# Kernel optimization log

Hardware: AMD Instinct MI355X
Metric: run time of the kernel (lower is better)

Reference implementation:

```python
import jax, jax.numpy as jnp
import numpy as np

B, V, L, H, E, META = 2048, 4096, 10, 512, 256, 15
TAU = 1.2
SOS = 0
EOS = 0


def setup_inputs() -> dict:
    key = jax.random.key(0)
    ks = jax.random.split(key, 8)
    hidden_state = jax.random.normal(ks[0], (B, META), jnp.float32)
    W_in = jax.random.normal(ks[1], (META, H), jnp.float32) * 0.1
    b_in = jnp.zeros((H,), jnp.float32)
    embedding = jax.random.normal(ks[2], (V, E), jnp.float32) * 0.1
    W_ih = jax.random.normal(ks[3], (4 * H, E), jnp.float32) * (1.0 / np.sqrt(E))
    W_hh = jax.random.normal(ks[4], (4 * H, H), jnp.float32) * (1.0 / np.sqrt(H))
    b_ih = jnp.zeros((4 * H,), jnp.float32)
    # forget-gate bias initialized to 1 (reset_parameters)
    b_hh = jnp.zeros((4 * H,), jnp.float32).at[H:2 * H].set(1.0)
    W_out = jax.random.normal(ks[5], (H, V), jnp.float32) * 0.02
    b_out = jnp.zeros((V,), jnp.float32)
    u = jax.random.uniform(ks[6], (L, B, V), jnp.float32, 1e-8, 1.0 - 1e-8)
    gumbel = -jnp.log(-jnp.log(u))
    return {"hidden_state": hidden_state, "W_in": W_in, "b_in": b_in,
            "embedding": embedding, "W_ih": W_ih, "W_hh": W_hh,
            "b_ih": b_ih, "b_hh": b_hh, "W_out": W_out, "b_out": b_out,
            "gumbel": gumbel}


def reference(hidden_state, W_in, b_in, embedding, W_ih, W_hh, b_ih, b_hh,
              W_out, b_out, gumbel):
    initial_length = L + 1
    h0 = hidden_state @ W_in + b_in              # [B,H] input_module (meta)
    c0 = jnp.zeros_like(h0)
    tok0 = jnp.zeros((B, V), jnp.float32).at[:, SOS].set(1.0)  # one-hot sos
    sl0 = jnp.full((B,), initial_length, jnp.int32)

    def step(carry, xs):
        h, c, tok, sl = carry
        i, g = xs
        emb = tok @ embedding                                  # [B,E]
        gates = emb @ W_ih.T + b_ih + h @ W_hh.T + b_hh        # [B,4H]
        ig, fg, gg, og = jnp.split(gates, 4, axis=1)
        c = jax.nn.sigmoid(fg) * c + jax.nn.sigmoid(ig) * jnp.tanh(gg)
        h = jax.nn.sigmoid(og) * jnp.tanh(c)
        logits = h @ W_out + b_out                             # [B,V]
        logp = jax.nn.log_softmax(logits, axis=1)
        p = jnp.exp(logp)
        ent = -jnp.sum(p * logp, axis=1)                       # Categorical entropy
        # gumbel_softmax(p, tau, hard=True): softmax((log p + g)/tau), straight-through
        y = jax.nn.softmax((logp + g) / TAU, axis=1)
        hard = jax.nn.one_hot(jnp.argmax(y, axis=1), V, dtype=y.dtype)
        tok_new = jax.lax.stop_gradient(hard - y) + y
        mask = (hard[:, EOS] == 1.0) & (sl == initial_length)
        sl = jnp.where(mask, i + 2, sl)  # seq_pos = i+1, set to seq_pos+1
        return (h, c, tok_new, sl), (tok_new, emb, ent)

    (_, _, _, seq_lengths), (toks, embeds, ents) = jax.lax.scan(
        step, (h0, c0, tok0, sl0), (jnp.arange(L, dtype=jnp.int32), gumbel))
    output = jnp.concatenate([tok0[:, None, :], jnp.transpose(toks, (1, 0, 2))], axis=1)  # [B,L+1,V]
    embeds_out = jnp.transpose(embeds, (1, 0, 2))              # [B,L,E]
    entropy = jnp.mean(jnp.sum(ents, axis=0)) / L
    sentence_probability = jnp.zeros((B, V), jnp.float32)      # only filled in eval mode
    return output, seq_lengths, entropy, embeds_out, sentence_probability
```

## Files before the change

kernel.cpp:

```cpp
#include <hip/hip_runtime.h>
#include <hip/hip_bf16.h>
#include <math.h>

typedef unsigned short u16;
typedef __attribute__((ext_vector_type(8))) short bf16x8;
typedef __attribute__((ext_vector_type(4))) float f32x4;

#define B_    2048
#define V_    4096
#define L_    10
#define H_    512
#define E_    256
#define META_ 15
#define H4_   2048
#define W6_   (H4_ + V_)
#define EOS_  0
#define INIT_LEN_ (L_ + 1)

constexpr size_t OUT_SL  = (size_t)B_ * (L_ + 1) * V_;
constexpr size_t OUT_ENT = OUT_SL + B_;
constexpr size_t OUT_EMB = OUT_ENT + 1;
constexpr size_t OUT_SP  = OUT_EMB + (size_t)B_ * L_ * E_;

constexpr size_t WS_E2G     = 0;
constexpr size_t WS_LOGITS  = WS_E2G    + (size_t)V_ * H4_;
constexpr size_t WS_G       = WS_LOGITS + (size_t)B_ * V_;
constexpr size_t WS_C       = WS_G      + (size_t)B_ * H4_;
constexpr size_t WS_F32_END = WS_C      + (size_t)B_ * H_;
constexpr size_t U_W6_HI    = 0;
constexpr size_t U_W6_LO    = U_W6_HI + (size_t)W6_ * H_;
constexpr size_t U_HHI      = U_W6_LO + (size_t)W6_ * H_;
constexpr size_t U_HLO      = U_HHI   + (size_t)B_ * H_;
constexpr size_t U_END      = U_HLO   + (size_t)B_ * H_;

__device__ __forceinline__ u16 f2bf(float f) {
    union { __hip_bfloat16 b; u16 u; } cv; cv.b = __float2bfloat16(f); return cv.u;
}
__device__ __forceinline__ float bf2f(u16 u) {
    union { u16 u; __hip_bfloat16 b; } cv; cv.u = u; return __bfloat162float(cv.b);
}

__device__ __forceinline__ void gld16(const u16* g, void* l) {
    __builtin_amdgcn_global_load_lds(
        (const __attribute__((address_space(1))) unsigned int*)g,
        (__attribute__((address_space(3))) unsigned int*)l, 16, 0, 0);
}

template <int EPI>
__global__ __launch_bounds__(256)
void gemm3(const u16* __restrict__ Ah, const u16* __restrict__ Al,
           const u16* __restrict__ Bh, const u16* __restrict__ Bl,
           float* __restrict__ C0, float* __restrict__ C1, int K,
           const float* __restrict__ bias0, const float* __restrict__ bias1,
           int xoff)
{
    __shared__ u16 As[2][128][32];
    __shared__ u16 Bs[2][128][32];
    const int tid  = threadIdx.x;
    const int lane = tid & 63;
    const int wave = tid >> 6;
    const int wm = wave >> 1, wn = wave & 1;

    const int nwg  = gridDim.x * gridDim.y;
    const int bid  = blockIdx.y * gridDim.x + blockIdx.x;
    const int w    = (bid & 7) * (nwg >> 3) + (bid >> 3);
    const int colb = w / gridDim.y + xoff;
    const int rowb = w % gridDim.y;
    const int col0 = colb * 128;
    const int row0 = rowb * 128;

    const int srow = tid >> 2;
    const int scol = (tid & 3) * 8;
    const size_t aoff = (size_t)(row0 + srow) * K + scol;
    const size_t boff = (size_t)(col0 + srow) * K + scol;
    const size_t skip = (size_t)64 * K;

    u16* lA0 = &As[0][0][0];
    u16* lA1 = &As[1][0][0];
    u16* lB0 = &Bs[0][0][0];
    u16* lB1 = &Bs[1][0][0];
    const int d0 = tid * 8;
    const int d1 = d0 + 2048;

    f32x4 acc[4][4] = {};
    const int fr = lane & 15;
    const int kq = lane >> 4;

    for (int k0 = 0; k0 < K; k0 += 32) {
        __syncthreads();
        gld16(Ah + aoff + k0,        lA0 + d0);
        gld16(Ah + aoff + k0 + skip, lA0 + d1);
        gld16(Al + aoff + k0,        lA1 + d0);
        gld16(Al + aoff + k0 + skip, lA1 + d1);
        gld16(Bh + boff + k0,        lB0 + d0);
        gld16(Bh + boff + k0 + skip, lB0 + d1);
        gld16(Bl + boff + k0,        lB1 + d0);
        gld16(Bl + boff + k0 + skip, lB1 + d1);
        __syncthreads();

        bf16x8 ah[4], al[4], bh[4], bl[4];
#pragma unroll
        for (int i = 0; i < 4; ++i) {
            ah[i] = *(const bf16x8*)&As[0][wm * 64 + i * 16 + fr][kq * 8];
            al[i] = *(const bf16x8*)&As[1][wm * 64 + i * 16 + fr][kq * 8];
            bh[i] = *(const bf16x8*)&Bs[0][wn * 64 + i * 16 + fr][kq * 8];
            bl[i] = *(const bf16x8*)&Bs[1][wn * 64 + i * 16 + fr][kq * 8];
        }
#pragma unroll
        for (int mi = 0; mi < 4; ++mi)
#pragma unroll
            for (int ni = 0; ni < 4; ++ni) {
                acc[mi][ni] = __builtin_amdgcn_mfma_f32_16x16x32_bf16(ah[mi], bh[ni], acc[mi][ni], 0, 0, 0);
                acc[mi][ni] = __builtin_amdgcn_mfma_f32_16x16x32_bf16(ah[mi], bl[ni], acc[mi][ni], 0, 0, 0);
                acc[mi][ni] = __builtin_amdgcn_mfma_f32_16x16x32_bf16(al[mi], bh[ni], acc[mi][ni], 0, 0, 0);
            }
    }

    const int cc0 = col0 + wn * 64 + fr;
    float* Cbase;
    int ldc, ccol;
    bool addBias;
    if (EPI == 0) {
        Cbase = C0; ldc = H4_; ccol = cc0; addBias = true;
    } else {
        const bool isG = (col0 < H4_);
        Cbase = isG ? C0 : C1;
        ldc   = isG ? H4_ : V_;
        ccol  = isG ? cc0 : cc0 - H4_;
        addBias = !isG;
    }
#pragma unroll
    for (int mi = 0; mi < 4; ++mi) {
#pragma unroll
        for (int r = 0; r < 4; ++r) {
            const int grow = row0 + wm * 64 + mi * 16 + kq * 4 + r;
            float* cp = Cbase + (size_t)grow * ldc + ccol;
#pragma unroll
            for (int ni = 0; ni < 4; ++ni) {
                float v = acc[mi][ni][r];
                if (EPI == 0) v += bias0[ccol + ni * 16] + bias1[ccol + ni * 16];
                if (EPI == 1 && addBias) v += bias0[ccol + ni * 16];
                cp[ni * 16] = v;
            }
        }
    }
}

__global__ __launch_bounds__(256)
void split_wout(const float* __restrict__ W_out, u16* __restrict__ hiT,
                u16* __restrict__ loT)
{
    __shared__ float t[32][33];
    const int v0 = blockIdx.x * 32, k0 = blockIdx.y * 32;
    const int x = threadIdx.x & 31, y = threadIdx.x >> 5;
    for (int yy = y; yy < 32; yy += 8)
        t[yy][x] = W_out[(size_t)(k0 + yy) * V_ + v0 + x];
    __syncthreads();
    for (int yy = y; yy < 32; yy += 8) {
        const float v = t[x][yy];
        const u16 h = f2bf(v);
        hiT[(size_t)(v0 + yy) * H_ + k0 + x] = h;
        loT[(size_t)(v0 + yy) * H_ + k0 + x] = f2bf(v - bf2f(h));
    }
}

__global__ __launch_bounds__(256)
void split_mat(const float* __restrict__ X, u16* __restrict__ hi,
               u16* __restrict__ lo)
{
    const int i = blockIdx.x * 256 + threadIdx.x;
    float4 v = ((const float4*)X)[i];
    const u16 h0 = f2bf(v.x), h1 = f2bf(v.y), h2 = f2bf(v.z), h3 = f2bf(v.w);
    ((ushort4*)hi)[i] = make_ushort4(h0, h1, h2, h3);
    ((ushort4*)lo)[i] = make_ushort4(f2bf(v.x - bf2f(h0)), f2bf(v.y - bf2f(h1)),
                                     f2bf(v.z - bf2f(h2)), f2bf(v.w - bf2f(h3)));
}

__global__ __launch_bounds__(256)
void h0_kernel(const float* __restrict__ hs, const float* __restrict__ W_in,
               const float* __restrict__ b_in, u16* __restrict__ h_hi,
               u16* __restrict__ h_lo, float* __restrict__ c)
{
    const int idx = blockIdx.x * 256 + threadIdx.x;
    const int b = idx >> 9, j = idx & 511;
    float acc = b_in[j];
#pragma unroll
    for (int e = 0; e < META_; ++e)
        acc = fmaf(hs[b * META_ + e], W_in[e * H_ + j], acc);
    const u16 hh = f2bf(acc);
    h_hi[idx] = hh;
    h_lo[idx] = f2bf(acc - bf2f(hh));
    c[idx] = 0.f;
}

__global__ __launch_bounds__(256)
void init_outputs(float* __restrict__ out, int* __restrict__ tok,
                  int* __restrict__ sl, float* __restrict__ ents)
{
    const int tid = blockIdx.x * 256 + threadIdx.x;
    {
        const int b = tid >> 10;
        const int q = tid & 1023;
        float4 z = make_float4(0.f, 0.f, 0.f, 0.f);
        if (q == 0) z.x = 1.0f;
        ((float4*)out)[(size_t)b * ((L_ + 1) * V_ / 4) + q] = z;
    }
    for (size_t t = tid; t < (size_t)B_ * V_; t += (size_t)gridDim.x * 256)
        out[OUT_SP + t] = 0.f;
    if (tid < B_) { tok[tid] = 0; sl[tid] = INIT_LEN_; ents[tid] = 0.f; }
}

__global__ __launch_bounds__(256)
void lstm_cell(const float* __restrict__ G, const float* __restrict__ e2g,
               u16* __restrict__ h_hi, u16* __restrict__ h_lo,
               float* __restrict__ c, const float* __restrict__ embedding,
               const int* __restrict__ tok, float* __restrict__ out, int step)
{
    const int idx = blockIdx.x * 256 + threadIdx.x;
    const int b = idx >> 9, j = idx & 511;
    const size_t g0 = (size_t)b * H4_;
    const size_t e0 = (size_t)tok[b] * H4_;
    const float ig = G[g0 + j]          + e2g[e0 + j];
    const float fg = G[g0 + H_ + j]     + e2g[e0 + H_ + j];
    const float gg = G[g0 + 2 * H_ + j] + e2g[e0 + 2 * H_ + j];
    const float og = G[g0 + 3 * H_ + j] + e2g[e0 + 3 * H_ + j];
    const float si = 1.f / (1.f + expf(-ig));
    const float sf = 1.f / (1.f + expf(-fg));
    const float so = 1.f / (1.f + expf(-og));
    const float cn = sf * c[idx] + si * tanhf(gg);
    c[idx] = cn;
    const float hv = so * tanhf(cn);
    const u16 hh = f2bf(hv);
    h_hi[idx] = hh;
    h_lo[idx] = f2bf(hv - bf2f(hh));
    if (j < E_)
        out[OUT_EMB + ((size_t)b * L_ + step) * E_ + j] =
            embedding[(size_t)tok[b] * E_ + j];
}

__global__ __launch_bounds__(256)
void softmax_step(const float* __restrict__ logits, const float* __restrict__ gumbel,
                  float* __restrict__ out, int* __restrict__ tok,
                  int* __restrict__ sl, float* __restrict__ ents, int step)
{
    const int b   = blockIdx.x;
    const int tid = threadIdx.x;
    const float* lrow = logits + (size_t)b * V_;
    const float* grow = gumbel + ((size_t)step * B_ + b) * V_;
    __shared__ float lsm[V_];
    __shared__ float red_m[4], red_bv[4], red_s[4], red_t[4];
    __shared__ int   red_bi[4];
    __shared__ float s_M;
    __shared__ int   s_bi;

    float m = -3.4e38f, bv = -3.4e38f;
    int bi = 0x7fffffff;
    for (int q = tid; q < V_ / 4; q += 256) {
        float4 l4 = ((const float4*)lrow)[q];
        float4 g4 = ((const float4*)grow)[q];
        ((float4*)lsm)[q] = l4;
        m = fmaxf(m, fmaxf(fmaxf(l4.x, l4.y), fmaxf(l4.z, l4.w)));
        float p; const int i4 = q * 4;
        p = l4.x + g4.x; if (p > bv) { bv = p; bi = i4; }
        p = l4.y + g4.y; if (p > bv) { bv = p; bi = i4 + 1; }
        p = l4.z + g4.z; if (p > bv) { bv = p; bi = i4 + 2; }
        p = l4.w + g4.w; if (p > bv) { bv = p; bi = i4 + 3; }
    }
#pragma unroll
    for (int off = 32; off > 0; off >>= 1) {
        m = fmaxf(m, __shfl_down(m, off));
        float obv = __shfl_down(bv, off);
        int   obi = __shfl_down(bi, off);
        if (obv > bv || (obv == bv && obi < bi)) { bv = obv; bi = obi; }
    }
    const int wave = tid >> 6, lane = tid & 63;
    if (lane == 0) { red_m[wave] = m; red_bv[wave] = bv; red_bi[wave] = bi; }
    __syncthreads();
    if (tid == 0) {
        m = red_m[0]; bv = red_bv[0]; bi = red_bi[0];
        for (int w = 1; w < 4; ++w) {
            m = fmaxf(m, red_m[w]);
            if (red_bv[w] > bv || (red_bv[w] == bv && red_bi[w] < bi)) {
                bv = red_bv[w]; bi = red_bi[w];
            }
        }
        s_M = m; s_bi = bi;
    }
    __syncthreads();
    const float M = s_M;
    const int amax = s_bi;

    float s = 0.f, t = 0.f;
    for (int q = tid; q < V_; q += 256) {
        const float l = lsm[q];
        const float e = __expf(l - M);
        s += e; t += e * l;
    }
#pragma unroll
    for (int off = 32; off > 0; off >>= 1) {
        s += __shfl_down(s, off);
        t += __shfl_down(t, off);
    }
    if (lane == 0) { red_s[wave] = s; red_t[wave] = t; }

    float* orow = out + ((size_t)b * (L_ + 1) + step + 1) * V_;
    const float4 z4 = make_float4(0.f, 0.f, 0.f, 0.f);
    for (int q = tid; q < V_ / 4; q += 256) ((float4*)orow)[q] = z4;
    __syncthreads();
    if (tid == 0) {
        const float ss = red_s[0] + red_s[1] + red_s[2] + red_s[3];
        const float tt = red_t[0] + red_t[1] + red_t[2] + red_t[3];
        const float ent = (M + logf(ss)) - tt / ss;
        ents[b] += ent;
        orow[amax] = 1.0f;
        tok[b] = amax;
        if (amax == EOS_ && sl[b] == INIT_LEN_) sl[b] = step + 2;
    }
}

__global__ __launch_bounds__(256)
void finalize(const int* __restrict__ sl, const float* __restrict__ ents,
              float* __restrict__ out)
{
    const int tid = threadIdx.x;
    float s = 0.f;
    for (int b = tid; b < B_; b += 256) {
        s += ents[b];
        out[OUT_SL + b] = (float)sl[b];
    }
    __shared__ float red[4];
#pragma unroll
    for (int off = 32; off > 0; off >>= 1) s += __shfl_down(s, off);
    if ((tid & 63) == 0) red[tid >> 6] = s;
    __syncthreads();
    if (tid == 0)
        out[OUT_ENT] = (red[0] + red[1] + red[2] + red[3]) / (float)B_ / (float)L_;
}

extern "C" void kernel_launch(void* const* d_in, const int* in_sizes, int n_in,
                              void* d_out, int out_size, void* d_ws, size_t ws_size,
                              hipStream_t stream)
{
    const float* hidden    = (const float*)d_in[0];
    const float* W_in      = (const float*)d_in[1];
    const float* b_in      = (const float*)d_in[2];
    const float* embedding = (const float*)d_in[3];
    const float* W_ih      = (const float*)d_in[4];
    const float* W_hh      = (const float*)d_in[5];
    const float* b_ih      = (const float*)d_in[6];
    const float* b_hh      = (const float*)d_in[7];
    const float* W_out     = (const float*)d_in[8];
    const float* b_out     = (const float*)d_in[9];
    const float* gumbel    = (const float*)d_in[10];
    float* out = (float*)d_out;

    float* ws    = (float*)d_ws;
    float* E2G   = ws + WS_E2G;
    float* logit = ws + WS_LOGITS;
    float* G     = ws + WS_G;
    float* c     = ws + WS_C;
    u16*   wsu   = (u16*)(ws + WS_F32_END);
    u16* w6_hi   = wsu + U_W6_HI;
    u16* w6_lo   = wsu + U_W6_LO;
    u16* h_hi    = wsu + U_HHI;
    u16* h_lo    = wsu + U_HLO;
    int* tok     = (int*)(wsu + U_END);
    int* sl      = tok + B_;
    float* ents  = (float*)(sl + B_);
    u16* emb_hi  = (u16*)logit;
    u16* emb_lo  = emb_hi + (size_t)V_ * E_;
    u16* wih_hi  = emb_lo + (size_t)V_ * E_;
    u16* wih_lo  = wih_hi + (size_t)H4_ * E_;

    split_mat<<<(H4_ * H_ / 4) / 256, 256, 0, stream>>>(W_hh, w6_hi, w6_lo);
    split_wout<<<dim3(V_ / 32, H_ / 32), 256, 0, stream>>>(
        W_out, w6_hi + (size_t)H4_ * H_, w6_lo + (size_t)H4_ * H_);
    split_mat<<<(V_ * E_ / 4) / 256, 256, 0, stream>>>(embedding, emb_hi, emb_lo);
    split_mat<<<(H4_ * E_ / 4) / 256, 256, 0, stream>>>(W_ih, wih_hi, wih_lo);
    h0_kernel<<<(B_ * H_) / 256, 256, 0, stream>>>(hidden, W_in, b_in, h_hi, h_lo, c);
    init_outputs<<<(B_ * V_ / 4) / 256, 256, 0, stream>>>(out, tok, sl, ents);
    gemm3<0><<<dim3(H4_ / 128, V_ / 128), 256, 0, stream>>>(
        emb_hi, emb_lo, wih_hi, wih_lo, E2G, nullptr, E_, b_ih, b_hh, 0);
    gemm3<1><<<dim3(H4_ / 128, B_ / 128), 256, 0, stream>>>(
        h_hi, h_lo, w6_hi, w6_lo, G, logit, H_, b_out, nullptr, 0);

    for (int i = 0; i < L_; ++i) {
        lstm_cell<<<(B_ * H_) / 256, 256, 0, stream>>>(G, E2G, h_hi, h_lo, c,
                                                       embedding, tok, out, i);
        if (i < L_ - 1) {
            gemm3<1><<<dim3(W6_ / 128, B_ / 128), 256, 0, stream>>>(
                h_hi, h_lo, w6_hi, w6_lo, G, logit, H_, b_out, nullptr, 0);
        } else {
            gemm3<1><<<dim3(V_ / 128, B_ / 128), 256, 0, stream>>>(
                h_hi, h_lo, w6_hi, w6_lo, G, logit, H_, b_out, nullptr, H4_ / 128);
        }
        softmax_step<<<B_, 256, 0, stream>>>(logit, gumbel, out, tok, sl, ents, i);
    }
    finalize<<<1, 256, 0, stream>>>(sl, ents, out);
}
```

Measured before the change: 865.1 us.

## Replace split-bf16 GEMM with 256x256-tile kernel over concatenated hi/lo K dimension

```diff
diff --git a/kernel.cpp b/kernel.cpp
--- a/kernel.cpp
+++ b/kernel.cpp
@@ -13,7 +13,8 @@
 #define E_    256
 #define META_ 15
 #define H4_   2048
-#define W6_   (H4_ + V_)
+#define KT_   1536
+#define NT_   48
 #define EOS_  0
 #define INIT_LEN_ (L_ + 1)
 
@@ -27,11 +28,9 @@
 constexpr size_t WS_G       = WS_LOGITS + (size_t)B_ * V_;
 constexpr size_t WS_C       = WS_G      + (size_t)B_ * H4_;
 constexpr size_t WS_F32_END = WS_C      + (size_t)B_ * H_;
-constexpr size_t U_W6_HI    = 0;
-constexpr size_t U_W6_LO    = U_W6_HI + (size_t)W6_ * H_;
-constexpr size_t U_HHI      = U_W6_LO + (size_t)W6_ * H_;
-constexpr size_t U_HLO      = U_HHI   + (size_t)B_ * H_;
-constexpr size_t U_END      = U_HLO   + (size_t)B_ * H_;
+constexpr size_t U_B6       = 0;
+constexpr size_t U_HP       = U_B6 + (size_t)6144 * KT_;
+constexpr size_t U_END      = U_HP + (size_t)B_ * KT_;
 
 __device__ __forceinline__ u16 f2bf(float f) {
     union { __hip_bfloat16 b; u16 u; } cv; cv.b = __float2bfloat16(f); return cv.u;
@@ -39,11 +38,164 @@
 __device__ __forceinline__ float bf2f(u16 u) {
     union { u16 u; __hip_bfloat16 b; } cv; cv.u = u; return __bfloat162float(cv.b);
 }
-
 __device__ __forceinline__ void gld16(const u16* g, void* l) {
     __builtin_amdgcn_global_load_lds(
         (const __attribute__((address_space(1))) unsigned int*)g,
         (__attribute__((address_space(3))) unsigned int*)l, 16, 0, 0);
+}
+
+__device__ __forceinline__ size_t b6_addr(int col, int k) {
+    const int p = col >> 8, row = col & 255, kt = k >> 5, s = (k >> 3) & 3, e = k & 7;
+    return (size_t)(p * NT_ + kt) * 8192 + s * 2048 + row * 8 + e;
+}
+
+__global__ __launch_bounds__(512, 1)
+void gemm8(const u16* __restrict__ Ag, const u16* __restrict__ B6,
+           float* __restrict__ G, float* __restrict__ LOG,
+           const float* __restrict__ bias, int xoff)
+{
+    __shared__ u16 As[2][8192];
+    __shared__ u16 Bs[2][8192];
+    const int tid  = threadIdx.x;
+    const int lane = tid & 63;
+    const int wave = tid >> 6;
+    const int wr = wave >> 2, wc = wave & 3;
+    const int fr = lane & 15, kq = lane >> 4;
+
+    const int nwg = gridDim.x * gridDim.y;
+    const int bid = blockIdx.y * gridDim.x + blockIdx.x;
+    const int w   = (bid & 7) * (nwg >> 3) + (bid >> 3);
+    const int colb = (w >> 3) + xoff;
+    const int row0 = (w & 7) * 256;
+    const int col0 = colb * 256;
+
+    const u16* Asrc = Ag + (size_t)(row0 + (tid & 255)) * KT_ + (tid >> 8) * 8;
+    const u16* Bsrc = B6 + (size_t)colb * (NT_ * 8192) + tid * 8;
+    const int dst0 = tid * 8;
+
+    const int abase = kq * 2048 + (wr * 128 + fr) * 8;
+    const int bbase = kq * 2048 + (wc * 64 + fr) * 8;
+
+    f32x4 acc[8][4] = {};
+    bf16x8 aF[8], bF[4], aN[8], bN[4];
+
+#define STAGE(buf, kt) do {                                    \
+    gld16(Asrc + (kt) * 32,        &As[buf][dst0]);            \
+    gld16(Asrc + (kt) * 32 + 16,   &As[buf][dst0 + 4096]);     \
+    gld16(Bsrc + (kt) * 8192,        &Bs[buf][dst0]);          \
+    gld16(Bsrc + (kt) * 8192 + 4096, &Bs[buf][dst0 + 4096]);   \
+  } while (0)
+
+    STAGE(0, 0);
+    STAGE(1, 1);
+    asm volatile("s_waitcnt vmcnt(4)\ns_barrier" ::: "memory");
+    {
+        const u16* ap = &As[0][abase];
+        const u16* bp = &Bs[0][bbase];
+#pragma unroll
+        for (int m = 0; m < 8; ++m) aF[m] = *(const bf16x8*)(ap + m * 128);
+#pragma unroll
+        for (int n = 0; n < 4; ++n) bF[n] = *(const bf16x8*)(bp + n * 128);
+    }
+
+#define BODY(T, AF, BF, AN, BN) do {                                          \
+    const int cur = (T) & 1;                                                  \
+    __builtin_amdgcn_s_setprio(1);                                            \
+    _Pragma("unroll")                                                         \
+    for (int m = 0; m < 8; ++m) {                                             \
+      acc[m][0] = __builtin_amdgcn_mfma_f32_16x16x32_bf16(AF[m], BF[0], acc[m][0], 0, 0, 0); \
+      acc[m][1] = __builtin_amdgcn_mfma_f32_16x16x32_bf16(AF[m], BF[1], acc[m][1], 0, 0, 0); \
+    }                                                                         \
+    __builtin_amdgcn_s_setprio(0);                                            \
+    asm volatile("s_waitcnt lgkmcnt(0)\ns_barrier" ::: "memory");             \
+    { int t2 = (T) + 2; if (t2 >= NT_) t2 = (T);                              \
+      STAGE(cur, t2); }                                                       \
+    __builtin_amdgcn_s_setprio(1);                                            \
+    _Pragma("unroll")                                                         \
+    for (int m = 0; m < 8; ++m)                                               \
+      acc[m][2] = __builtin_amdgcn_mfma_f32_16x16x32_bf16(AF[m], BF[2], acc[m][2], 0, 0, 0); \
+    __builtin_amdgcn_s_setprio(0);                                            \
+    asm volatile("s_waitcnt vmcnt(4)\ns_barrier" ::: "memory");               \
+    { const u16* ap = &As[cur ^ 1][abase];                                    \
+      const u16* bp = &Bs[cur ^ 1][bbase];                                    \
+      _Pragma("unroll")                                                       \
+      for (int m = 0; m < 8; ++m) AN[m] = *(const bf16x8*)(ap + m * 128);     \
+      _Pragma("unroll")                                                       \
+      for (int n = 0; n < 4; ++n) BN[n] = *(const bf16x8*)(bp + n * 128); }   \
+    __builtin_amdgcn_s_setprio(1);                                            \
+    _Pragma("unroll")                                                         \
+    for (int m = 0; m < 8; ++m)                                               \
+      acc[m][3] = __builtin_amdgcn_mfma_f32_16x16x32_bf16(AF[m], BF[3], acc[m][3], 0, 0, 0); \
+    __builtin_amdgcn_s_setprio(0);                                            \
+  } while (0)
+
+    for (int t = 0; t < NT_; t += 2) {
+        BODY(t,     aF, bF, aN, bN);
+        BODY(t + 1, aN, bN, aF, bF);
+    }
+#undef BODY
+#undef STAGE
+
+    const bool isG = (col0 < H4_);
+    float* Cb   = isG ? G : LOG;
+    const int ldc  = isG ? H4_ : V_;
+    const int cadj = isG ? 0 : H4_;
+    const int cbase = col0 - cadj + wc * 64 + fr;
+#pragma unroll
+    for (int m = 0; m < 8; ++m) {
+#pragma unroll
+        for (int r = 0; r < 4; ++r) {
+            const int grow = row0 + wr * 128 + m * 16 + kq * 4 + r;
+            float* cp = Cb + (size_t)grow * ldc + cbase;
+#pragma unroll
+            for (int n = 0; n < 4; ++n) {
+                float v = acc[m][n][r];
+                if (!isG) v += bias[cbase + n * 16];
+                cp[n * 16] = v;
+            }
+        }
+    }
+}
+
+__global__ __launch_bounds__(256)
+void repack_whh(const float* __restrict__ W_hh, u16* __restrict__ B6)
+{
+    const int c0 = blockIdx.x * 32, k0 = blockIdx.y * 64;
+    const int cc = threadIdx.x & 31, kg = threadIdx.x >> 5;
+    const int col = c0 + cc;
+#pragma unroll
+    for (int e = 0; e < 8; ++e) {
+        const int kp = k0 + kg * 8 + e;
+        const float v = W_hh[(size_t)col * H_ + kp];
+        const u16 h = f2bf(v);
+        const u16 l = f2bf(v - bf2f(h));
+        B6[b6_addr(col, kp)]          = h;
+        B6[b6_addr(col, 512 + kp)]    = h;
+        B6[b6_addr(col, 1024 + kp)]   = l;
+    }
+}
+
+__global__ __launch_bounds__(256)
+void repack_wout(const float* __restrict__ W_out, u16* __restrict__ B6)
+{
+    __shared__ float t[64][33];
+    const int c0 = blockIdx.x * 32, k0 = blockIdx.y * 64;
+    const int x = threadIdx.x & 31, y = threadIdx.x >> 5;
+    for (int yy = y; yy < 64; yy += 8)
+        t[yy][x] = W_out[(size_t)(k0 + yy) * V_ + c0 + x];
+    __syncthreads();
+    const int cc = threadIdx.x & 31, kg = threadIdx.x >> 5;
+    const int col = 2048 + c0 + cc;
+#pragma unroll
+    for (int e = 0; e < 8; ++e) {
+        const int kp = k0 + kg * 8 + e;
+        const float v = t[kp - k0][cc];
+        const u16 h = f2bf(v);
+        const u16 l = f2bf(v - bf2f(h));
+        B6[b6_addr(col, kp)]        = h;
+        B6[b6_addr(col, 512 + kp)]  = h;
+        B6[b6_addr(col, 1024 + kp)] = l;
+    }
 }
 
 template <int EPI>
@@ -60,7 +212,6 @@
     const int lane = tid & 63;
     const int wave = tid >> 6;
     const int wm = wave >> 1, wn = wave & 1;
-
     const int nwg  = gridDim.x * gridDim.y;
     const int bid  = blockIdx.y * gridDim.x + blockIdx.x;
     const int w    = (bid & 7) * (nwg >> 3) + (bid >> 3);
@@ -117,50 +268,16 @@
     }
 
     const int cc0 = col0 + wn * 64 + fr;
-    float* Cbase;
-    int ldc, ccol;
-    bool addBias;
-    if (EPI == 0) {
-        Cbase = C0; ldc = H4_; ccol = cc0; addBias = true;
-    } else {
-        const bool isG = (col0 < H4_);
-        Cbase = isG ? C0 : C1;
-        ldc   = isG ? H4_ : V_;
-        ccol  = isG ? cc0 : cc0 - H4_;
-        addBias = !isG;
-    }
 #pragma unroll
     for (int mi = 0; mi < 4; ++mi) {
 #pragma unroll
         for (int r = 0; r < 4; ++r) {
             const int grow = row0 + wm * 64 + mi * 16 + kq * 4 + r;
-            float* cp = Cbase + (size_t)grow * ldc + ccol;
-#pragma unroll
-            for (int ni = 0; ni < 4; ++ni) {
-                float v = acc[mi][ni][r];
-                if (EPI == 0) v += bias0[ccol + ni * 16] + bias1[ccol + ni * 16];
-                if (EPI == 1 && addBias) v += bias0[ccol + ni * 16];
-                cp[ni * 16] = v;
-            }
+            float* cp = C0 + (size_t)grow * H4_ + cc0;
+#pragma unroll
+            for (int ni = 0; ni < 4; ++ni)
+                cp[ni * 16] = acc[mi][ni][r] + bias0[cc0 + ni * 16] + bias1[cc0 + ni * 16];
         }
-    }
-}
-
-__global__ __launch_bounds__(256)
-void split_wout(const float* __restrict__ W_out, u16* __restrict__ hiT,
-                u16* __restrict__ loT)
-{
-    __shared__ float t[32][33];
-    const int v0 = blockIdx.x * 32, k0 = blockIdx.y * 32;
-    const int x = threadIdx.x & 31, y = threadIdx.x >> 5;
-    for (int yy = y; yy < 32; yy += 8)
-        t[yy][x] = W_out[(size_t)(k0 + yy) * V_ + v0 + x];
-    __syncthreads();
-    for (int yy = y; yy < 32; yy += 8) {
-        const float v = t[x][yy];
-        const u16 h = f2bf(v);
-        hiT[(size_t)(v0 + yy) * H_ + k0 + x] = h;
-        loT[(size_t)(v0 + yy) * H_ + k0 + x] = f2bf(v - bf2f(h));
     }
 }
 
@@ -178,8 +295,8 @@
 
 __global__ __launch_bounds__(256)
 void h0_kernel(const float* __restrict__ hs, const float* __restrict__ W_in,
-               const float* __restrict__ b_in, u16* __restrict__ h_hi,
-               u16* __restrict__ h_lo, float* __restrict__ c)
+               const float* __restrict__ b_in, u16* __restrict__ hp,
+               float* __restrict__ c)
 {
     const int idx = blockIdx.x * 256 + threadIdx.x;
     const int b = idx >> 9, j = idx & 511;
@@ -188,8 +305,9 @@
     for (int e = 0; e < META_; ++e)
         acc = fmaf(hs[b * META_ + e], W_in[e * H_ + j], acc);
     const u16 hh = f2bf(acc);
-    h_hi[idx] = hh;
-    h_lo[idx] = f2bf(acc - bf2f(hh));
+    const u16 hl = f2bf(acc - bf2f(hh));
+    u16* row = hp + (size_t)b * KT_;
+    row[j] = hh; row[512 + j] = hl; row[1024 + j] = hh;
     c[idx] = 0.f;
 }
 
@@ -212,9 +330,9 @@
 
 __global__ __launch_bounds__(256)
 void lstm_cell(const float* __restrict__ G, const float* __restrict__ e2g,
-               u16* __restrict__ h_hi, u16* __restrict__ h_lo,
-               float* __restrict__ c, const float* __restrict__ embedding,
-               const int* __restrict__ tok, float* __restrict__ out, int step)
+               u16* __restrict__ hp, float* __restrict__ c,
+               const float* __restrict__ embedding, const int* __restrict__ tok,
+               float* __restrict__ out, int step)
 {
     const int idx = blockIdx.x * 256 + threadIdx.x;
     const int b = idx >> 9, j = idx & 511;
@@ -231,8 +349,9 @@
     c[idx] = cn;
     const float hv = so * tanhf(cn);
     const u16 hh = f2bf(hv);
-    h_hi[idx] = hh;
-    h_lo[idx] = f2bf(hv - bf2f(hh));
+    const u16 hl = f2bf(hv - bf2f(hh));
+    u16* row = hp + (size_t)b * KT_;
+    row[j] = hh; row[512 + j] = hl; row[1024 + j] = hh;
     if (j < E_)
         out[OUT_EMB + ((size_t)b * L_ + step) * E_ + j] =
             embedding[(size_t)tok[b] * E_ + j];
@@ -360,10 +479,8 @@
     float* G     = ws + WS_G;
     float* c     = ws + WS_C;
     u16*   wsu   = (u16*)(ws + WS_F32_END);
-    u16* w6_hi   = wsu + U_W6_HI;
-    u16* w6_lo   = wsu + U_W6_LO;
-    u16* h_hi    = wsu + U_HHI;
-    u16* h_lo    = wsu + U_HLO;
+    u16* B6      = wsu + U_B6;
+    u16* hp      = wsu + U_HP;
     int* tok     = (int*)(wsu + U_END);
     int* sl      = tok + B_;
     float* ents  = (float*)(sl + B_);
@@ -372,27 +489,23 @@
     u16* wih_hi  = emb_lo + (size_t)V_ * E_;
     u16* wih_lo  = wih_hi + (size_t)H4_ * E_;
 
-    split_mat<<<(H4_ * H_ / 4) / 256, 256, 0, stream>>>(W_hh, w6_hi, w6_lo);
-    split_wout<<<dim3(V_ / 32, H_ / 32), 256, 0, stream>>>(
-        W_out, w6_hi + (size_t)H4_ * H_, w6_lo + (size_t)H4_ * H_);
+    repack_whh<<<dim3(H4_ / 32, H_ / 64), 256, 0, stream>>>(W_hh, B6);
+    repack_wout<<<dim3(V_ / 32, H_ / 64), 256, 0, stream>>>(W_out, B6);
     split_mat<<<(V_ * E_ / 4) / 256, 256, 0, stream>>>(embedding, emb_hi, emb_lo);
     split_mat<<<(H4_ * E_ / 4) / 256, 256, 0, stream>>>(W_ih, wih_hi, wih_lo);
-    h0_kernel<<<(B_ * H_) / 256, 256, 0, stream>>>(hidden, W_in, b_in, h_hi, h_lo, c);
+    h0_kernel<<<(B_ * H_) / 256, 256, 0, stream>>>(hidden, W_in, b_in, hp, c);
     init_outputs<<<(B_ * V_ / 4) / 256, 256, 0, stream>>>(out, tok, sl, ents);
     gemm3<0><<<dim3(H4_ / 128, V_ / 128), 256, 0, stream>>>(
         emb_hi, emb_lo, wih_hi, wih_lo, E2G, nullptr, E_, b_ih, b_hh, 0);
-    gemm3<1><<<dim3(H4_ / 128, B_ / 128), 256, 0, stream>>>(
-        h_hi, h_lo, w6_hi, w6_lo, G, logit, H_, b_out, nullptr, 0);
+    gemm8<<<dim3(8, 8), 512, 0, stream>>>(hp, B6, G, logit, b_out, 0);
 
     for (int i = 0; i < L_; ++i) {
-        lstm_cell<<<(B_ * H_) / 256, 256, 0, stream>>>(G, E2G, h_hi, h_lo, c,
+        lstm_cell<<<(B_ * H_) / 256, 256, 0, stream>>>(G, E2G, hp, c,
                                                        embedding, tok, out, i);
         if (i < L_ - 1) {
-            gemm3<1><<<dim3(W6_ / 128, B_ / 128), 256, 0, stream>>>(
-                h_hi, h_lo, w6_hi, w6_lo, G, logit, H_, b_out, nullptr, 0);
+            gemm8<<<dim3(24, 8), 512, 0, stream>>>(hp, B6, G, logit, b_out, 0);
         } else {
-            gemm3<1><<<dim3(V_ / 128, B_ / 128), 256, 0, stream>>>(
-                h_hi, h_lo, w6_hi, w6_lo, G, logit, H_, b_out, nullptr, H4_ / 128);
+            gemm8<<<dim3(16, 8), 512, 0, stream>>>(hp, B6, G, logit, b_out, 8);
         }
         softmax_step<<<B_, 256, 0, stream>>>(logit, gumbel, out, tok, sl, ents, i);
     }
```

New measurement: 1.222 ms. 1.41x slower.

## Fuse softmax partial reductions into GEMM epilogue and merge with LSTM cell

Applied to the files above, without the earlier changes.

```diff
diff --git a/kernel.cpp b/kernel.cpp
--- a/kernel.cpp
+++ b/kernel.cpp
@@ -23,10 +23,10 @@
 constexpr size_t OUT_SP  = OUT_EMB + (size_t)B_ * L_ * E_;
 
 constexpr size_t WS_E2G     = 0;
-constexpr size_t WS_LOGITS  = WS_E2G    + (size_t)V_ * H4_;
-constexpr size_t WS_G       = WS_LOGITS + (size_t)B_ * V_;
-constexpr size_t WS_C       = WS_G      + (size_t)B_ * H4_;
-constexpr size_t WS_F32_END = WS_C      + (size_t)B_ * H_;
+constexpr size_t WS_SCR     = WS_E2G + (size_t)V_ * H4_;
+constexpr size_t WS_G       = WS_SCR + (size_t)B_ * V_;
+constexpr size_t WS_C       = WS_G   + (size_t)B_ * H4_;
+constexpr size_t WS_F32_END = WS_C   + (size_t)B_ * H_;
 constexpr size_t U_W6_HI    = 0;
 constexpr size_t U_W6_LO    = U_W6_HI + (size_t)W6_ * H_;
 constexpr size_t U_HHI      = U_W6_LO + (size_t)W6_ * H_;
@@ -50,9 +50,9 @@
 __global__ __launch_bounds__(256)
 void gemm3(const u16* __restrict__ Ah, const u16* __restrict__ Al,
            const u16* __restrict__ Bh, const u16* __restrict__ Bl,
-           float* __restrict__ C0, float* __restrict__ C1, int K,
+           float* __restrict__ C0, float* __restrict__ part, int K,
            const float* __restrict__ bias0, const float* __restrict__ bias1,
-           int xoff)
+           const float* __restrict__ gumbel, int step, int xoff)
 {
     __shared__ u16 As[2][128][32];
     __shared__ u16 Bs[2][128][32];
@@ -116,33 +116,138 @@
             }
     }
 
-    const int cc0 = col0 + wn * 64 + fr;
-    float* Cbase;
-    int ldc, ccol;
-    bool addBias;
-    if (EPI == 0) {
-        Cbase = C0; ldc = H4_; ccol = cc0; addBias = true;
+    if (EPI == 0 || col0 < H4_) {
+        const int cc0 = col0 + wn * 64 + fr;
+#pragma unroll
+        for (int mi = 0; mi < 4; ++mi) {
+#pragma unroll
+            for (int r = 0; r < 4; ++r) {
+                const int grow = row0 + wm * 64 + mi * 16 + kq * 4 + r;
+                float* cp = C0 + (size_t)grow * H4_ + cc0;
+#pragma unroll
+                for (int ni = 0; ni < 4; ++ni) {
+                    float v = acc[mi][ni][r];
+                    if (EPI == 0) v += bias0[cc0 + ni * 16] + bias1[cc0 + ni * 16];
+                    cp[ni * 16] = v;
+                }
+            }
+        }
     } else {
-        const bool isG = (col0 < H4_);
-        Cbase = isG ? C0 : C1;
-        ldc   = isG ? H4_ : V_;
-        ccol  = isG ? cc0 : cc0 - H4_;
-        addBias = !isG;
-    }
-#pragma unroll
-    for (int mi = 0; mi < 4; ++mi) {
-#pragma unroll
-        for (int r = 0; r < 4; ++r) {
-            const int grow = row0 + wm * 64 + mi * 16 + kq * 4 + r;
-            float* cp = Cbase + (size_t)grow * ldc + ccol;
-#pragma unroll
-            for (int ni = 0; ni < 4; ++ni) {
-                float v = acc[mi][ni][r];
-                if (EPI == 0) v += bias0[ccol + ni * 16] + bias1[ccol + ni * 16];
-                if (EPI == 1 && addBias) v += bias0[ccol + ni * 16];
-                cp[ni * 16] = v;
+        const int vbase = (col0 - H4_) + wn * 64 + fr;
+        const int grp   = ((col0 - H4_) >> 6) + wn;
+        const float* gum = gumbel + (size_t)step * B_ * V_;
+#pragma unroll
+        for (int mi = 0; mi < 4; ++mi) {
+#pragma unroll
+            for (int r = 0; r < 4; ++r) {
+                const int grow = row0 + wm * 64 + mi * 16 + kq * 4 + r;
+                const float* gr = gum + (size_t)grow * V_ + vbase;
+                float l[4], gv[4];
+#pragma unroll
+                for (int ni = 0; ni < 4; ++ni) l[ni] = acc[mi][ni][r] + bias0[vbase + ni * 16];
+#pragma unroll
+                for (int ni = 0; ni < 4; ++ni) gv[ni] = gr[ni * 16];
+                float lm = fmaxf(fmaxf(l[0], l[1]), fmaxf(l[2], l[3]));
+#pragma unroll
+                for (int d = 1; d < 16; d <<= 1) lm = fmaxf(lm, __shfl_xor(lm, d));
+                float s = 0.f, t = 0.f;
+#pragma unroll
+                for (int ni = 0; ni < 4; ++ni) {
+                    const float e = __expf(l[ni] - lm);
+                    s += e; t += l[ni] * e;
+                }
+                float bv = l[0] + gv[0];
+                int   bi = vbase;
+#pragma unroll
+                for (int ni = 1; ni < 4; ++ni) {
+                    const float p = l[ni] + gv[ni];
+                    const int ci = vbase + ni * 16;
+                    if (p > bv) { bv = p; bi = ci; }
+                }
+#pragma unroll
+                for (int d = 1; d < 16; d <<= 1) {
+                    s += __shfl_xor(s, d);
+                    t += __shfl_xor(t, d);
+                    const float ob = __shfl_xor(bv, d);
+                    const int   oi = __shfl_xor(bi, d);
+                    if (ob > bv || (ob == bv && oi < bi)) { bv = ob; bi = oi; }
+                }
+                if (fr == 0) {
+                    float* pp = part + ((size_t)grow * 64 + grp) * 8;
+                    pp[0] = lm; pp[1] = s; pp[2] = t; pp[3] = bv;
+                    *(int*)(pp + 4) = bi;
+                }
             }
         }
+    }
+}
+
+template <bool LAST>
+__global__ __launch_bounds__(256)
+void step_merge(const float* __restrict__ part, const float* __restrict__ G,
+                const float* __restrict__ e2g, const float* __restrict__ embedding,
+                u16* __restrict__ h_hi, u16* __restrict__ h_lo,
+                float* __restrict__ c, float* __restrict__ out,
+                int* __restrict__ sl, float* __restrict__ ents, int step)
+{
+    const int b = blockIdx.x, tid = threadIdx.x;
+    __shared__ float sM, sS, sT;
+    __shared__ int   sAmax;
+    if (tid < 64) {
+        const float* pp = part + ((size_t)b * 64 + tid) * 8;
+        float m = pp[0], s = pp[1], t = pp[2], bv = pp[3];
+        int bi = *(const int*)(pp + 4);
+#pragma unroll
+        for (int d = 1; d < 64; d <<= 1) {
+            const float om = __shfl_xor(m, d), os = __shfl_xor(s, d), ot = __shfl_xor(t, d);
+            const float ob = __shfl_xor(bv, d);
+            const int   oi = __shfl_xor(bi, d);
+            const float M = fmaxf(m, om);
+            const float e0 = __expf(m - M), e1 = __expf(om - M);
+            s = s * e0 + os * e1;
+            t = t * e0 + ot * e1;
+            m = M;
+            if (ob > bv || (ob == bv && oi < bi)) { bv = ob; bi = oi; }
+        }
+        if (tid == 0) { sM = m; sS = s; sT = t; sAmax = bi; }
+    }
+    __syncthreads();
+    const int amax = sAmax;
+
+    float* orow = out + ((size_t)b * (L_ + 1) + step + 1) * V_;
+    const float4 z4 = make_float4(0.f, 0.f, 0.f, 0.f);
+    for (int q = tid; q < V_ / 4; q += 256) ((float4*)orow)[q] = z4;
+    __syncthreads();
+    if (tid == 0) {
+        orow[amax] = 1.0f;
+        ents[b] += (sM + logf(sS)) - sT / sS;
+        if (amax == EOS_ && sl[b] == INIT_LEN_) sl[b] = step + 2;
+    }
+
+    if (!LAST) {
+        const float* Gr = G + (size_t)b * H4_;
+        const float* er = e2g + (size_t)amax * H4_;
+#pragma unroll
+        for (int jj = 0; jj < 2; ++jj) {
+            const int j = tid + jj * 256;
+            const float ig = Gr[j]          + er[j];
+            const float fg = Gr[H_ + j]     + er[H_ + j];
+            const float gg = Gr[2 * H_ + j] + er[2 * H_ + j];
+            const float og = Gr[3 * H_ + j] + er[3 * H_ + j];
+            const float si = 1.f / (1.f + expf(-ig));
+            const float sf = 1.f / (1.f + expf(-fg));
+            const float so = 1.f / (1.f + expf(-og));
+            const size_t idx = (size_t)b * H_ + j;
+            const float cn = sf * c[idx] + si * tanhf(gg);
+            c[idx] = cn;
+            const float hv = so * tanhf(cn);
+            const u16 hh = f2bf(hv);
+            h_hi[idx] = hh;
+            h_lo[idx] = f2bf(hv - bf2f(hh));
+        }
+        if (tid < E_)
+            out[OUT_EMB + ((size_t)b * L_ + step + 1) * E_ + tid] =
+                embedding[(size_t)amax * E_ + tid];
     }
 }
 
@@ -239,86 +344,6 @@
 }
 
 __global__ __launch_bounds__(256)
-void softmax_step(const float* __restrict__ logits, const float* __restrict__ gumbel,
-                  float* __restrict__ out, int* __restrict__ tok,
-                  int* __restrict__ sl, float* __restrict__ ents, int step)
-{
-    const int b   = blockIdx.x;
-    const int tid = threadIdx.x;
-    const float* lrow = logits + (size_t)b * V_;
-    const float* grow = gumbel + ((size_t)step * B_ + b) * V_;
-    __shared__ float lsm[V_];
-    __shared__ float red_m[4], red_bv[4], red_s[4], red_t[4];
-    __shared__ int   red_bi[4];
-    __shared__ float s_M;
-    __shared__ int   s_bi;
-
-    float m = -3.4e38f, bv = -3.4e38f;
-    int bi = 0x7fffffff;
-    for (int q = tid; q < V_ / 4; q += 256) {
-        float4 l4 = ((const float4*)lrow)[q];
-        float4 g4 = ((const float4*)grow)[q];
-        ((float4*)lsm)[q] = l4;
-        m = fmaxf(m, fmaxf(fmaxf(l4.x, l4.y), fmaxf(l4.z, l4.w)));
-        float p; const int i4 = q * 4;
-        p = l4.x + g4.x; if (p > bv) { bv = p; bi = i4; }
-        p = l4.y + g4.y; if (p > bv) { bv = p; bi = i4 + 1; }
-        p = l4.z + g4.z; if (p > bv) { bv = p; bi = i4 + 2; }
-        p = l4.w + g4.w; if (p > bv) { bv = p; bi = i4 + 3; }
-    }
-#pragma unroll
-    for (int off = 32; off > 0; off >>= 1) {
-        m = fmaxf(m, __shfl_down(m, off));
-        float obv = __shfl_down(bv, off);
-        int   obi = __shfl_down(bi, off);
-        if (obv > bv || (obv == bv && obi < bi)) { bv = obv; bi = obi; }
-    }
-    const int wave = tid >> 6, lane = tid & 63;
-    if (lane == 0) { red_m[wave] = m; red_bv[wave] = bv; red_bi[wave] = bi; }
-    __syncthreads();
-    if (tid == 0) {
-        m = red_m[0]; bv = red_bv[0]; bi = red_bi[0];
-        for (int w = 1; w < 4; ++w) {
-            m = fmaxf(m, red_m[w]);
-            if (red_bv[w] > bv || (red_bv[w] == bv && red_bi[w] < bi)) {
-                bv = red_bv[w]; bi = red_bi[w];
-            }
-        }
-        s_M = m; s_bi = bi;
-    }
-    __syncthreads();
-    const float M = s_M;
-    const int amax = s_bi;
-
-    float s = 0.f, t = 0.f;
-    for (int q = tid; q < V_; q += 256) {
-        const float l = lsm[q];
-        const float e = __expf(l - M);
-        s += e; t += e * l;
-    }
-#pragma unroll
-    for (int off = 32; off > 0; off >>= 1) {
-        s += __shfl_down(s, off);
-        t += __shfl_down(t, off);
-    }
-    if (lane == 0) { red_s[wave] = s; red_t[wave] = t; }
-
-    float* orow = out + ((size_t)b * (L_ + 1) + step + 1) * V_;
-    const float4 z4 = make_float4(0.f, 0.f, 0.f, 0.f);
-    for (int q = tid; q < V_ / 4; q += 256) ((float4*)orow)[q] = z4;
-    __syncthreads();
-    if (tid == 0) {
-        const float ss = red_s[0] + red_s[1] + red_s[2] + red_s[3];
-        const float tt = red_t[0] + red_t[1] + red_t[2] + red_t[3];
-        const float ent = (M + logf(ss)) - tt / ss;
-        ents[b] += ent;
-        orow[amax] = 1.0f;
-        tok[b] = amax;
-        if (amax == EOS_ && sl[b] == INIT_LEN_) sl[b] = step + 2;
-    }
-}
-
-__global__ __launch_bounds__(256)
 void finalize(const int* __restrict__ sl, const float* __restrict__ ents,
               float* __restrict__ out)
 {
@@ -356,7 +381,7 @@
 
     float* ws    = (float*)d_ws;
     float* E2G   = ws + WS_E2G;
-    float* logit = ws + WS_LOGITS;
+    float* scr   = ws + WS_SCR;
     float* G     = ws + WS_G;
     float* c     = ws + WS_C;
     u16*   wsu   = (u16*)(ws + WS_F32_END);
@@ -367,10 +392,11 @@
     int* tok     = (int*)(wsu + U_END);
     int* sl      = tok + B_;
     float* ents  = (float*)(sl + B_);
-    u16* emb_hi  = (u16*)logit;
+    u16* emb_hi  = (u16*)scr;
     u16* emb_lo  = emb_hi + (size_t)V_ * E_;
     u16* wih_hi  = emb_lo + (size_t)V_ * E_;
     u16* wih_lo  = wih_hi + (size_t)H4_ * E_;
+    float* part  = scr;
 
     split_mat<<<(H4_ * H_ / 4) / 256, 256, 0, stream>>>(W_hh, w6_hi, w6_lo);
     split_wout<<<dim3(V_ / 32, H_ / 32), 256, 0, stream>>>(
@@ -380,21 +406,27 @@
     h0_kernel<<<(B_ * H_) / 256, 256, 0, stream>>>(hidden, W_in, b_in, h_hi, h_lo, c);
     init_outputs<<<(B_ * V_ / 4) / 256, 256, 0, stream>>>(out, tok, sl, ents);
     gemm3<0><<<dim3(H4_ / 128, V_ / 128), 256, 0, stream>>>(
-        emb_hi, emb_lo, wih_hi, wih_lo, E2G, nullptr, E_, b_ih, b_hh, 0);
+        emb_hi, emb_lo, wih_hi, wih_lo, E2G, nullptr, E_, b_ih, b_hh,
+        nullptr, 0, 0);
     gemm3<1><<<dim3(H4_ / 128, B_ / 128), 256, 0, stream>>>(
-        h_hi, h_lo, w6_hi, w6_lo, G, logit, H_, b_out, nullptr, 0);
+        h_hi, h_lo, w6_hi, w6_lo, G, part, H_, b_out, nullptr, gumbel, 0, 0);
+    lstm_cell<<<(B_ * H_) / 256, 256, 0, stream>>>(G, E2G, h_hi, h_lo, c,
+                                                   embedding, tok, out, 0);
 
     for (int i = 0; i < L_; ++i) {
-        lstm_cell<<<(B_ * H_) / 256, 256, 0, stream>>>(G, E2G, h_hi, h_lo, c,
-                                                       embedding, tok, out, i);
         if (i < L_ - 1) {
             gemm3<1><<<dim3(W6_ / 128, B_ / 128), 256, 0, stream>>>(
-                h_hi, h_lo, w6_hi, w6_lo, G, logit, H_, b_out, nullptr, 0);
+                h_hi, h_lo, w6_hi, w6_lo, G, part, H_, b_out, nullptr,
+                gumbel, i, 0);
+            step_merge<false><<<B_, 256, 0, stream>>>(
+                part, G, E2G, embedding, h_hi, h_lo, c, out, sl, ents, i);
         } else {
             gemm3<1><<<dim3(V_ / 128, B_ / 128), 256, 0, stream>>>(
-                h_hi, h_lo, w6_hi, w6_lo, G, logit, H_, b_out, nullptr, H4_ / 128);
-        }
-        softmax_step<<<B_, 256, 0, stream>>>(logit, gumbel, out, tok, sl, ents, i);
+                h_hi, h_lo, w6_hi, w6_lo, G, part, H_, b_out, nullptr,
+                gumbel, i, H4_ / 128);
+            step_merge<true><<<B_, 256, 0, stream>>>(
+                part, G, E2G, embedding, h_hi, h_lo, c, out, sl, ents, i);
+        }
     }
     finalize<<<1, 256, 0, stream>>>(sl, ents, out);
 }
```

Result: slower. 1.055 ms (+22.0%).
